# Performance work log

Measured on AMD Instinct MI355X. Metric: run time of the kernel, lower is better.

Reference implementation:

```python
import jax, jax.numpy as jnp
import numpy as np

N = 8192
E = 131072
C_IN = 256
C_OUT = 256


def setup_inputs() -> dict:
    key = jax.random.key(0)
    k1, k2, k3, k4 = jax.random.split(key, 4)
    x = jax.random.normal(k1, (N, C_IN), dtype=jnp.float32)
    edge_index = jax.random.randint(k2, (2, E), 0, N, dtype=jnp.int64)
    # nn.Linear params (PyTorch layout: W is (out, in))
    bound = 1.0 / np.sqrt(C_IN)
    W = jax.random.uniform(k3, (C_OUT, C_IN), minval=-bound, maxval=bound, dtype=jnp.float32)
    b_lin = jax.random.uniform(k4, (C_OUT,), minval=-bound, maxval=bound, dtype=jnp.float32)
    bias = jnp.zeros((C_OUT,), dtype=jnp.float32)  # extra learned bias parameter
    return {"x": x, "W": W, "b_lin": b_lin, "bias": bias, "edge_index": edge_index}


def reference(x, W, b_lin, bias, edge_index):
    n = x.shape[0]
    # Dense adjacency built by scatter ASSIGNMENT (duplicate edges collapse to 1.0),
    # matching torch's adj[e0, e1] = 1.0
    adj = jnp.zeros((n, n), dtype=x.dtype).at[edge_index[0], edge_index[1]].set(1.0)
    # adj = adj + eye (diagonal entries can become 2.0 if self-loop edge exists)
    diag = jnp.arange(n)
    adj = adj.at[diag, diag].add(1.0)
    deg = adj.sum(axis=1)
    # pow(deg, -0.5) with inf -> 0 (deg == 0 case)
    deg_inv_sqrt = jnp.where(deg > 0, 1.0 / jnp.sqrt(deg), 0.0)
    # symmetric normalization: D^-1/2 A D^-1/2
    norm = deg_inv_sqrt[:, None] * adj * deg_inv_sqrt[None, :]
    out = norm @ x                      # (N, C_in)
    out = out @ W.T + b_lin + bias      # (N, C_out)
    return out
```

## Files before the change

kernel.cpp:

```cpp
#include <hip/hip_runtime.h>
#include <stdint.h>

#define N_NODES 8192
#define CH      256
#define NWORDS  256
#define BM_WORDS (N_NODES * NWORDS)
#define LIST_CAP 192

typedef short bf16x8 __attribute__((ext_vector_type(8)));
typedef float f32x4  __attribute__((ext_vector_type(4)));

static __device__ __forceinline__ unsigned short f2bf(float f) {
    union { float f; uint32_t u; } v; v.f = f;
    uint32_t r = v.u + 0x7fff + ((v.u >> 16) & 1);
    return (unsigned short)(r >> 16);
}
static __device__ __forceinline__ uint32_t pack2bf(float lo, float hi) {
    return (uint32_t)f2bf(lo) | ((uint32_t)f2bf(hi) << 16);
}
static __device__ __forceinline__ float bfbits_lo(uint32_t u) {
    union { uint32_t u; float f; } v; v.u = u << 16; return v.f;
}
static __device__ __forceinline__ float bfbits_hi(uint32_t u) {
    union { uint32_t u; float f; } v; v.u = u & 0xffff0000u; return v.f;
}

__global__ void k_edges(const int* __restrict__ ei, uint32_t* __restrict__ bm, int E) {
    int e = blockIdx.x * blockDim.x + threadIdx.x;
    if (e >= E) return;
    int r = ei[e];
    int c = ei[E + e];
    atomicOr(&bm[r * NWORDS + (c >> 5)], 1u << (c & 31));
}

__global__ __launch_bounds__(64) void k_deg_y(const uint32_t* __restrict__ bm,
                                              const float* __restrict__ x,
                                              const float* __restrict__ W,
                                              uint32_t* __restrict__ y,
                                              uint32_t* __restrict__ Wb) {
    int lane = threadIdx.x;
    if (blockIdx.x < N_NODES) {
        int row = blockIdx.x;
        uint4 w4 = ((const uint4*)(bm + (size_t)row * NWORDS))[lane];
        int cnt = __popc(w4.x) + __popc(w4.y) + __popc(w4.z) + __popc(w4.w);
        #pragma unroll
        for (int off = 1; off < 64; off <<= 1) cnt += __shfl_xor(cnt, off);
        float di = rsqrtf((float)(cnt + 1));
        float4 xv = ((const float4*)(x + (size_t)row * CH))[lane];
        uint2 o;
        o.x = pack2bf(di * xv.x, di * xv.y);
        o.y = pack2bf(di * xv.z, di * xv.w);
        ((uint2*)y)[row * 64 + lane] = o;
    } else {
        int i = (blockIdx.x - N_NODES) * 256 + lane * 4;
        float4 wv = *(const float4*)(W + i);
        uint2 o;
        o.x = pack2bf(wv.x, wv.y);
        o.y = pack2bf(wv.z, wv.w);
        *(uint2*)(Wb + i / 2) = o;
    }
}

__global__ __launch_bounds__(1024) void k_agg_gemm(
    const uint32_t* __restrict__ bm, const uint32_t* __restrict__ y,
    const unsigned short* __restrict__ Wb,
    const float* __restrict__ b1, const float* __restrict__ b2,
    float* __restrict__ out)
{
    const int tid  = threadIdx.x;
    const int bid  = blockIdx.x;
    const int lane = tid & 63;
    const int wid  = tid >> 6;

    __shared__ uint2 s_o1[32 * 66];
    __shared__ __align__(8) unsigned short s_list[16][LIST_CAP];

    const uint2* ys = (const uint2*)y;

    #pragma unroll
    for (int rr = 0; rr < 2; ++rr) {
        int rloc = wid * 2 + rr;
        int row  = bid * 32 + rloc;
        uint4 w4 = ((const uint4*)(bm + (size_t)row * NWORDS))[lane];
        int mycnt = __popc(w4.x) + __popc(w4.y) + __popc(w4.z) + __popc(w4.w);
        int pre = mycnt;
        #pragma unroll
        for (int off = 1; off < 64; off <<= 1) {
            int n = __shfl_up(pre, off);
            if (lane >= off) pre += n;
        }
        int total = __shfl(pre, 63);
        int p = pre - mycnt;
        uint32_t wrd[4] = {w4.x, w4.y, w4.z, w4.w};
        #pragma unroll
        for (int i = 0; i < 4; ++i) {
            uint32_t w = wrd[i];
            int basebit = lane * 128 + i * 32;
            while (w) {
                int b = __ffs(w) - 1;
                if (p < LIST_CAP) s_list[wid][p] = (unsigned short)(basebit + b);
                ++p;
                w &= (w - 1);
            }
        }
        float di = rsqrtf((float)(total + 1));

        uint2 d = ys[row * 64 + lane];
        float a0 = bfbits_lo(d.x), a1 = bfbits_hi(d.x);
        float a2 = bfbits_lo(d.y), a3 = bfbits_hi(d.y);
        int cnt = total < LIST_CAP ? total : LIST_CAP;
        int k = 0;
        for (; k + 8 <= cnt; k += 8) {
            uint2 dv[8];
            #pragma unroll
            for (int u = 0; u < 8; ++u)
                dv[u] = ys[(int)s_list[wid][k + u] * 64 + lane];
            #pragma unroll
            for (int u = 0; u < 8; ++u) {
                a0 += bfbits_lo(dv[u].x); a1 += bfbits_hi(dv[u].x);
                a2 += bfbits_lo(dv[u].y); a3 += bfbits_hi(dv[u].y);
            }
        }
        for (; k < cnt; ++k) {
            uint2 dd = ys[(int)s_list[wid][k] * 64 + lane];
            a0 += bfbits_lo(dd.x); a1 += bfbits_hi(dd.x);
            a2 += bfbits_lo(dd.y); a3 += bfbits_hi(dd.y);
        }
        uint2 o;
        o.x = pack2bf(di * a0, di * a1);
        o.y = pack2bf(di * a2, di * a3);
        s_o1[rloc * 66 + lane] = o;
    }
    __syncthreads();

    {
        int rowHalf  = wid & 1;
        int colGroup = wid >> 1;
        int m16  = lane & 15;
        int quad = lane >> 4;
        int rloc_a = rowHalf * 16 + m16;
        f32x4 acc0 = {0.f, 0.f, 0.f, 0.f};
        f32x4 acc1 = {0.f, 0.f, 0.f, 0.f};
        #pragma unroll
        for (int k0 = 0; k0 < CH; k0 += 32) {
            uint4 av = *(const uint4*)&s_o1[rloc_a * 66 + (k0 >> 2) + quad * 2];
            bf16x8 af = __builtin_bit_cast(bf16x8, av);
            const unsigned short* w0 = Wb + (size_t)(colGroup * 32 + m16) * CH + k0 + quad * 8;
            bf16x8 bv0 = *(const bf16x8*)w0;
            acc0 = __builtin_amdgcn_mfma_f32_16x16x32_bf16(af, bv0, acc0, 0, 0, 0);
            bf16x8 bv1 = *(const bf16x8*)(w0 + 16 * CH);
            acc1 = __builtin_amdgcn_mfma_f32_16x16x32_bf16(af, bv1, acc1, 0, 0, 0);
        }
        int rowB = bid * 32 + rowHalf * 16 + quad * 4;
        int col0 = colGroup * 32 + m16;
        float bb0 = b1[col0] + b2[col0];
        float bb1 = b1[col0 + 16] + b2[col0 + 16];
        #pragma unroll
        for (int r = 0; r < 4; ++r)
            out[(size_t)(rowB + r) * CH + col0] = acc0[r] + bb0;
        #pragma unroll
        for (int r = 0; r < 4; ++r)
            out[(size_t)(rowB + r) * CH + col0 + 16] = acc1[r] + bb1;
    }
}

extern "C" void kernel_launch(void* const* d_in, const int* in_sizes, int n_in,
                              void* d_out, int out_size, void* d_ws, size_t ws_size,
                              hipStream_t stream) {
    const float* x   = (const float*)d_in[0];
    const float* W   = (const float*)d_in[1];
    const float* b1  = (const float*)d_in[2];
    const float* b2  = (const float*)d_in[3];
    const int*   ei  = (const int*)d_in[4];
    int E = in_sizes[4] / 2;
    float* out = (float*)d_out;

    uint8_t* ws = (uint8_t*)d_ws;
    uint32_t* bm = (uint32_t*)ws;
    uint32_t* y  = (uint32_t*)(ws + (8u << 20));
    uint32_t* Wb = (uint32_t*)(ws + (12u << 20));

    hipMemsetAsync(bm, 0, (size_t)BM_WORDS * 4, stream);
    k_edges<<<(E + 255) / 256, 256, 0, stream>>>(ei, bm, E);
    k_deg_y<<<N_NODES + 256, 64, 0, stream>>>(bm, x, W, y, Wb);
    k_agg_gemm<<<N_NODES / 32, 1024, 0, stream>>>(bm, y, (const unsigned short*)Wb,
                                                  b1, b2, out);
}
```

Baseline: 99.11 us.

## Build per-row neighbor lists during edge insertion instead of rescanning bitmap

```diff
diff --git a/kernel.cpp b/kernel.cpp
--- a/kernel.cpp
+++ b/kernel.cpp
@@ -25,34 +25,38 @@
     union { uint32_t u; float f; } v; v.u = u & 0xffff0000u; return v.f;
 }
 
-__global__ void k_edges(const int* __restrict__ ei, uint32_t* __restrict__ bm, int E) {
+__global__ void k_edges(const int* __restrict__ ei, uint32_t* __restrict__ bm,
+                        int* __restrict__ cnt, unsigned short* __restrict__ nlist,
+                        int E) {
     int e = blockIdx.x * blockDim.x + threadIdx.x;
     if (e >= E) return;
     int r = ei[e];
     int c = ei[E + e];
-    atomicOr(&bm[r * NWORDS + (c >> 5)], 1u << (c & 31));
+    uint32_t bit = 1u << (c & 31);
+    uint32_t old = atomicOr(&bm[r * NWORDS + (c >> 5)], bit);
+    if (!(old & bit)) {
+        int p = atomicAdd(&cnt[r], 1);
+        if (p < LIST_CAP) nlist[(size_t)r * LIST_CAP + p] = (unsigned short)c;
+    }
 }
 
-__global__ __launch_bounds__(64) void k_deg_y(const uint32_t* __restrict__ bm,
-                                              const float* __restrict__ x,
-                                              const float* __restrict__ W,
-                                              uint32_t* __restrict__ y,
-                                              uint32_t* __restrict__ Wb) {
-    int lane = threadIdx.x;
-    if (blockIdx.x < N_NODES) {
-        int row = blockIdx.x;
-        uint4 w4 = ((const uint4*)(bm + (size_t)row * NWORDS))[lane];
-        int cnt = __popc(w4.x) + __popc(w4.y) + __popc(w4.z) + __popc(w4.w);
-        #pragma unroll
-        for (int off = 1; off < 64; off <<= 1) cnt += __shfl_xor(cnt, off);
-        float di = rsqrtf((float)(cnt + 1));
+__global__ __launch_bounds__(256) void k_y(const int* __restrict__ cnt,
+                                           const float* __restrict__ x,
+                                           const float* __restrict__ W,
+                                           uint32_t* __restrict__ y,
+                                           uint32_t* __restrict__ Wb) {
+    int tid = threadIdx.x;
+    if (blockIdx.x < N_NODES / 4) {
+        int lane = tid & 63;
+        int row  = blockIdx.x * 4 + (tid >> 6);
+        float di = rsqrtf((float)(cnt[row] + 1));
         float4 xv = ((const float4*)(x + (size_t)row * CH))[lane];
         uint2 o;
         o.x = pack2bf(di * xv.x, di * xv.y);
         o.y = pack2bf(di * xv.z, di * xv.w);
         ((uint2*)y)[row * 64 + lane] = o;
     } else {
-        int i = (blockIdx.x - N_NODES) * 256 + lane * 4;
+        int i = (blockIdx.x - N_NODES / 4) * 1024 + tid * 4;
         float4 wv = *(const float4*)(W + i);
         uint2 o;
         o.x = pack2bf(wv.x, wv.y);
@@ -62,8 +66,8 @@
 }
 
 __global__ __launch_bounds__(1024) void k_agg_gemm(
-    const uint32_t* __restrict__ bm, const uint32_t* __restrict__ y,
-    const unsigned short* __restrict__ Wb,
+    const int* __restrict__ cnt, const unsigned short* __restrict__ nlist,
+    const uint32_t* __restrict__ y, const unsigned short* __restrict__ Wb,
     const float* __restrict__ b1, const float* __restrict__ b2,
     float* __restrict__ out)
 {
@@ -73,7 +77,7 @@
     const int wid  = tid >> 6;
 
     __shared__ uint2 s_o1[32 * 66];
-    __shared__ __align__(8) unsigned short s_list[16][LIST_CAP];
+    __shared__ unsigned short s_list[16][2][LIST_CAP];
 
     const uint2* ys = (const uint2*)y;
 
@@ -81,48 +85,32 @@
     for (int rr = 0; rr < 2; ++rr) {
         int rloc = wid * 2 + rr;
         int row  = bid * 32 + rloc;
-        uint4 w4 = ((const uint4*)(bm + (size_t)row * NWORDS))[lane];
-        int mycnt = __popc(w4.x) + __popc(w4.y) + __popc(w4.z) + __popc(w4.w);
-        int pre = mycnt;
-        #pragma unroll
-        for (int off = 1; off < 64; off <<= 1) {
-            int n = __shfl_up(pre, off);
-            if (lane >= off) pre += n;
-        }
-        int total = __shfl(pre, 63);
-        int p = pre - mycnt;
-        uint32_t wrd[4] = {w4.x, w4.y, w4.z, w4.w};
-        #pragma unroll
-        for (int i = 0; i < 4; ++i) {
-            uint32_t w = wrd[i];
-            int basebit = lane * 128 + i * 32;
-            while (w) {
-                int b = __ffs(w) - 1;
-                if (p < LIST_CAP) s_list[wid][p] = (unsigned short)(basebit + b);
-                ++p;
-                w &= (w - 1);
-            }
-        }
+        int total = cnt[row];
+        const unsigned short* lp = nlist + (size_t)row * LIST_CAP;
+        unsigned short* sl = s_list[wid][rr];
+        sl[lane]       = lp[lane];
+        sl[64 + lane]  = lp[64 + lane];
+        sl[128 + lane] = lp[128 + lane];
         float di = rsqrtf((float)(total + 1));
 
         uint2 d = ys[row * 64 + lane];
         float a0 = bfbits_lo(d.x), a1 = bfbits_hi(d.x);
         float a2 = bfbits_lo(d.y), a3 = bfbits_hi(d.y);
-        int cnt = total < LIST_CAP ? total : LIST_CAP;
+        int cn = total < LIST_CAP ? total : LIST_CAP;
         int k = 0;
-        for (; k + 8 <= cnt; k += 8) {
+        for (; k + 8 <= cn; k += 8) {
             uint2 dv[8];
             #pragma unroll
             for (int u = 0; u < 8; ++u)
-                dv[u] = ys[(int)s_list[wid][k + u] * 64 + lane];
+                dv[u] = ys[(int)sl[k + u] * 64 + lane];
             #pragma unroll
             for (int u = 0; u < 8; ++u) {
                 a0 += bfbits_lo(dv[u].x); a1 += bfbits_hi(dv[u].x);
                 a2 += bfbits_lo(dv[u].y); a3 += bfbits_hi(dv[u].y);
             }
         }
-        for (; k < cnt; ++k) {
-            uint2 dd = ys[(int)s_list[wid][k] * 64 + lane];
+        for (; k < cn; ++k) {
+            uint2 dd = ys[(int)sl[k] * 64 + lane];
             a0 += bfbits_lo(dd.x); a1 += bfbits_hi(dd.x);
             a2 += bfbits_lo(dd.y); a3 += bfbits_hi(dd.y);
         }
@@ -176,13 +164,15 @@
     float* out = (float*)d_out;
 
     uint8_t* ws = (uint8_t*)d_ws;
-    uint32_t* bm = (uint32_t*)ws;
-    uint32_t* y  = (uint32_t*)(ws + (8u << 20));
-    uint32_t* Wb = (uint32_t*)(ws + (12u << 20));
+    uint32_t* bm   = (uint32_t*)ws;
+    int* cnt       = (int*)(ws + (8u << 20));
+    uint32_t* y    = (uint32_t*)(ws + (9u << 20));
+    uint32_t* Wb   = (uint32_t*)(ws + (13u << 20));
+    unsigned short* nlist = (unsigned short*)(ws + (14u << 20));
 
-    hipMemsetAsync(bm, 0, (size_t)BM_WORDS * 4, stream);
-    k_edges<<<(E + 255) / 256, 256, 0, stream>>>(ei, bm, E);
-    k_deg_y<<<N_NODES + 256, 64, 0, stream>>>(bm, x, W, y, Wb);
-    k_agg_gemm<<<N_NODES / 32, 1024, 0, stream>>>(bm, y, (const unsigned short*)Wb,
+    hipMemsetAsync(bm, 0, (size_t)BM_WORDS * 4 + N_NODES * 4, stream);
+    k_edges<<<(E + 255) / 256, 256, 0, stream>>>(ei, bm, cnt, nlist, E);
+    k_y<<<N_NODES / 4 + 64, 256, 0, stream>>>(cnt, x, W, y, Wb);
+    k_agg_gemm<<<N_NODES / 32, 1024, 0, stream>>>(cnt, nlist, y, (const unsigned short*)Wb,
                                                   b1, b2, out);
 }
```

After: 103.1 us. 4.0% more time.
